# Kernel optimization log

Measured on AMD Instinct MI355X. Metric: run time of the kernel, lower is better.

The kernel has to match this reference:

```python
import jax, jax.numpy as jnp
import numpy as np

B, S, D, H = 2, 2048, 1024, 16
DEPTH = D // H

def setup_inputs() -> dict:
    key = jax.random.key(0)
    ks = jax.random.split(key, 6)
    sc = 0.02
    return {
        "x": jax.random.normal(ks[0], (B, S, D), dtype=jnp.float32),
        "mask": jnp.ones((S, S), dtype=jnp.int32),
        "wq": jax.random.normal(ks[1], (D, D), dtype=jnp.float32) * sc,
        "bq": jnp.zeros((D,), dtype=jnp.float32),
        "wk": jax.random.normal(ks[2], (D, D), dtype=jnp.float32) * sc,
        "bk": jnp.zeros((D,), dtype=jnp.float32),
        "wv": jax.random.normal(ks[3], (D, D), dtype=jnp.float32) * sc,
        "bv": jnp.zeros((D,), dtype=jnp.float32),
        "wo": jax.random.normal(ks[4], (D, D), dtype=jnp.float32) * sc,
        "bo": jnp.zeros((D,), dtype=jnp.float32),
    }

def _split_heads(t):
    # [B,S,D] -> [B,H,S,depth]
    b, s, _ = t.shape
    return t.reshape(b, s, H, DEPTH).transpose(0, 2, 1, 3)

def reference(x, mask, wq, bq, wk, bk, wv, bv, wo, bo):
    q = _split_heads(x @ wq + bq)
    k = _split_heads(x @ wk + bk)
    v = _split_heads(x @ wv + bv)
    scale = 1.0 / jnp.sqrt(jnp.asarray(DEPTH, x.dtype))
    scores = jnp.einsum('bhqd,bhkd->bhqk', q, k) * scale
    # Faithful to original: band_part(ones,-1,0) is the LOWER triangle
    # (incl. diagonal), and it is ADDED times -1e9 -> lower triangle masked.
    s_len = mask.shape[0]
    tri = jnp.tril(jnp.ones((s_len, s_len), dtype=x.dtype))
    scores = scores + tri * (-1e9)
    attn = jax.nn.softmax(scores, axis=-1)  # dropout is identity at inference
    out = jnp.einsum('bhqk,bhkd->bhqd', attn, v)
    out = out.transpose(0, 2, 1, 3).reshape(x.shape[0], -1, D)
    return out @ wo + bo
```

## Files before the change

### kernel.cpp

```cpp
#include <hip/hip_runtime.h>
#include <hip/hip_bf16.h>


using bf16   = __bf16;
using bf16x2 = __attribute__((ext_vector_type(2))) __bf16;
using bf16x4 = __attribute__((ext_vector_type(4))) __bf16;
using bf16x8 = __attribute__((ext_vector_type(8))) __bf16;
using f32x4  = __attribute__((ext_vector_type(4))) float;
using uintx2 = __attribute__((ext_vector_type(2))) unsigned int;
using uintx4 = __attribute__((ext_vector_type(4))) unsigned int;

__device__ __forceinline__ void load_lds16(const void* g, void* l) {
  __builtin_amdgcn_global_load_lds(
      (const __attribute__((address_space(1))) void*)g,
      (__attribute__((address_space(3))) void*)l, 16, 0, 0);
}

__device__ __forceinline__ unsigned int packbf(float a, float b) {
  bf16x2 v;
  v[0] = (bf16)a;
  v[1] = (bf16)b;
  return __builtin_bit_cast(unsigned int, v);
}

__device__ __forceinline__ void xchg_p(unsigned int u, unsigned int v, int hi,
                                       unsigned int& f, unsigned int& s) {
#if __has_builtin(__builtin_amdgcn_permlane32_swap) && \
    __has_builtin(__builtin_amdgcn_permlane16_swap)
  uintx2 ab = __builtin_amdgcn_permlane32_swap(u, v, false, false);
  uintx2 fs = __builtin_amdgcn_permlane16_swap(ab[0], ab[1], false, false);
  f = fs[0];
  s = fs[1];
#else
  unsigned int a = (hi < 2) ? u : (unsigned int)__shfl_xor((int)v, 32);
  unsigned int b = (hi < 2) ? (unsigned int)__shfl_xor((int)u, 32) : v;
  unsigned int a16 = (unsigned int)__shfl_xor((int)a, 16);
  unsigned int b16 = (unsigned int)__shfl_xor((int)b, 16);
  f = (hi & 1) ? b16 : a;
  s = (hi & 1) ? b : a16;
#endif
}

__global__ __launch_bounds__(256) void prep_kernel(
    const float* __restrict__ x, bf16* __restrict__ xb,
    const float* __restrict__ wq, const float* __restrict__ wk,
    const float* __restrict__ wv, const float* __restrict__ wo,
    bf16* __restrict__ wT) {
  const int t = threadIdx.x;
  int bid = blockIdx.x;
  if (bid < 4096) {
    const int i = (bid * 256 + t) * 4;
    const float4 v = *(const float4*)(x + i);
    bf16x4 o;
    o[0] = (bf16)v.x; o[1] = (bf16)v.y; o[2] = (bf16)v.z; o[3] = (bf16)v.w;
    *(bf16x4*)(xb + i) = o;
    return;
  }
  bid -= 4096;
  const int sel = bid >> 8;
  const float* w = (sel == 0) ? wq : (sel == 1) ? wk : (sel == 2) ? wv : wo;
  bf16* out = wT + (size_t)sel * 1048576;
  __shared__ float tile[64][65];
  const int n0 = (bid & 15) * 64;
  const int k0 = ((bid >> 4) & 15) * 64;
#pragma unroll
  for (int p = 0; p < 4; ++p) {
    const int row = p * 16 + (t >> 4);
    const int c4  = (t & 15) * 4;
    const float4 v = *(const float4*)&w[(size_t)(k0 + row) * 1024 + n0 + c4];
    tile[row][c4 + 0] = v.x; tile[row][c4 + 1] = v.y;
    tile[row][c4 + 2] = v.z; tile[row][c4 + 3] = v.w;
  }
  __syncthreads();
#pragma unroll
  for (int p = 0; p < 4; ++p) {
    const int rn = p * 16 + (t >> 4);
    const int c4 = (t & 15) * 4;
    bf16x4 o;
#pragma unroll
    for (int j = 0; j < 4; ++j) o[j] = (bf16)tile[c4 + j][rn];
    *(bf16x4*)&out[(size_t)(n0 + rn) * 1024 + k0 + c4] = o;
  }
}

template <int MODE>
__global__ __launch_bounds__(256, 2) void gemm_bt(
    const bf16* __restrict__ A, const bf16* __restrict__ Bt,
    const float* __restrict__ bias0, const float* __restrict__ bias1,
    const float* __restrict__ bias2, bf16* __restrict__ qf,
    bf16* __restrict__ kf, bf16* __restrict__ vt, float* __restrict__ fout,
    int Nblocks) {
  __shared__ __align__(16) char smem[32768];
  char* sA = smem;
  char* sB = smem + 16384;
  const int tid = threadIdx.x;
  const int lane = tid & 63;
  const int w = tid >> 6;
  const int wm = w >> 1, wn = w & 1;
  const int bid = blockIdx.x;
  const int m0 = (bid / Nblocks) * 128;
  const int n0 = (bid % Nblocks) * 128;

  const char* Ab = (const char*)A;
  const char* Bb = (const char*)Bt;
  size_t srcA[4], srcB[4];
#pragma unroll
  for (int it = 0; it < 4; ++it) {
    const int o = it * 4096 + tid * 16;
    const int r = o >> 7;
    const int cg = ((o >> 4) & 7) ^ (r & 7);
    srcA[it] = (size_t)(m0 + r) * 2048 + cg * 16;
    srcB[it] = (size_t)(n0 + r) * 2048 + cg * 16;
  }

  f32x4 acc[4][4] = {};

  for (int kt = 0; kt < 16; ++kt) {
    const size_t kb = (size_t)kt * 128;
#pragma unroll
    for (int it = 0; it < 4; ++it) {
      load_lds16(Ab + srcA[it] + kb, sA + it * 4096 + w * 1024);
      load_lds16(Bb + srcB[it] + kb, sB + it * 4096 + w * 1024);
    }
    asm volatile("s_waitcnt vmcnt(0)" ::: "memory");
    __syncthreads();
#pragma unroll
    for (int ks = 0; ks < 2; ++ks) {
      bf16x8 aF[4], bF[4];
      const int g = (lane >> 4) + 4 * ks;
#pragma unroll
      for (int i = 0; i < 4; ++i) {
        const int ra = wm * 64 + i * 16 + (lane & 15);
        aF[i] = *(const bf16x8*)(sA + ra * 128 + ((g ^ (ra & 7)) << 4));
        const int rb = wn * 64 + i * 16 + (lane & 15);
        bF[i] = *(const bf16x8*)(sB + rb * 128 + ((g ^ (rb & 7)) << 4));
      }
#pragma unroll
      for (int mi = 0; mi < 4; ++mi)
#pragma unroll
        for (int ni = 0; ni < 4; ++ni)
          acc[mi][ni] = __builtin_amdgcn_mfma_f32_16x16x32_bf16(
              aF[mi], bF[ni], acc[mi][ni], 0, 0, 0);
    }
    __syncthreads();
  }

  const int cn = lane & 15;
  const int gq = lane >> 4;
#pragma unroll
  for (int mi = 0; mi < 4; ++mi) {
#pragma unroll
    for (int ni = 0; ni < 4; ++ni) {
      const int n  = n0 + wn * 64 + ni * 16 + cn;
      const int mb = m0 + wm * 64 + mi * 16 + 4 * gq;
      const f32x4 v = acc[mi][ni];
      if (MODE == 0) {
        const float bias =
            (n < 1024) ? bias0[n] : ((n < 2048) ? bias1[n - 1024] : bias2[n - 2048]);
        if (n < 2048) {
          bf16* dst = (n < 1024) ? qf : kf;
          const int nn = n & 1023;
#pragma unroll
          for (int j = 0; j < 4; ++j)
            dst[(size_t)(mb + j) * 1024 + nn] = (bf16)(v[j] + bias);
        } else {
          const int nn = n - 2048;
          const int hh = nn >> 6, dd = nn & 63;
          const int bb = mb >> 11, ss = mb & 2047;
          bf16x4 pk;
#pragma unroll
          for (int j = 0; j < 4; ++j) pk[j] = (bf16)(v[j] + bias);
          *(bf16x4*)(vt + ((size_t)((bb * 16 + hh) * 64 + dd) * 2048 + ss)) = pk;
        }
      } else {
        const float bias = bias0[n];
#pragma unroll
        for (int j = 0; j < 4; ++j)
          fout[(size_t)(mb + j) * 1024 + n] = v[j] + bias;
      }
    }
  }
}

__global__ __launch_bounds__(256, 2) void attn_kernel(
    const bf16* __restrict__ qf, const bf16* __restrict__ kf,
    const bf16* __restrict__ vt, bf16* __restrict__ ao) {
  __shared__ __align__(16) char smem[32768];

  const int tid  = threadIdx.x;
  const int lane = tid & 63;
  const int hi   = lane >> 4;
  const int qlo  = lane & 15;
  const int w    = tid >> 6;
  const int ti = blockIdx.x >> 5;
  const int jq = (ti < 8) ? ti : 23 - ti;
  const int bh = blockIdx.x & 31;
  const int b = bh >> 4, h = bh & 15;

  const char* kbase = (const char*)kf + ((size_t)b * 2048) * 2048 + h * 128;
  const char* vbase = (const char*)vt + (size_t)bh * 262144;
  const char* qbb   = (const char*)qf + ((size_t)b * 2048) * 2048 + h * 128;

  const int sr  = tid >> 3;
  const int scg = (tid & 7) ^ (sr & 7);

  bf16x8 onesB;
#pragma unroll
  for (int i = 0; i < 8; ++i) onesB[i] = (bf16)1.0f;

  const int q0 = jq * 128;
  const int qb = q0 + w * 32;

  bf16x8 qA[2][2];
#pragma unroll
  for (int nt = 0; nt < 2; ++nt) {
    const char* qrow = qbb + (size_t)(qb + 16 * nt + qlo) * 2048;
#pragma unroll
    for (int ks = 0; ks < 2; ++ks) {
      qA[nt][ks] = *(const bf16x8*)(qrow + ks * 64 + hi * 16);
#pragma unroll
      for (int i = 0; i < 8; ++i)
        qA[nt][ks][i] = (bf16)(0.125f * (float)qA[nt][ks][i]);
    }
  }

  float m[2] = {-1e30f, -1e30f};
  f32x4 lacc[2] = {};
  f32x4 O[2][4] = {};

  const int nt_tiles = (2048 - q0) >> 6;

  {
    char* dK = smem + w * 1024;
    char* dV = smem + 16384 + w * 1024;
#pragma unroll
    for (int p = 0; p < 2; ++p) {
      load_lds16(kbase + (size_t)(q0 + sr + 32 * p) * 2048 + scg * 16,
                 dK + p * 4096);
      load_lds16(vbase + (size_t)(sr + 32 * p) * 4096 + (size_t)q0 * 2 +
                     scg * 16,
                 dV + p * 4096);
    }
  }
  __syncthreads();

  for (int it = 0; it < nt_tiles; ++it) {
    const int cur = it & 1;

    if (it + 1 < nt_tiles) {
      const int kn = q0 + it * 64 + 64;
      char* dK = smem + (cur ^ 1) * 8192 + w * 1024;
      char* dV = smem + 16384 + (cur ^ 1) * 8192 + w * 1024;
#pragma unroll
      for (int p = 0; p < 2; ++p) {
        load_lds16(kbase + (size_t)(kn + sr + 32 * p) * 2048 + scg * 16,
                   dK + p * 4096);
        load_lds16(vbase + (size_t)(sr + 32 * p) * 4096 + (size_t)kn * 2 +
                       scg * 16,
                   dV + p * 4096);
      }
    }
    const char* bK = smem + cur * 8192;
    const char* bV = smem + 16384 + cur * 8192;

    f32x4 sc[2][4] = {};
#pragma unroll
    for (int ks = 0; ks < 2; ++ks) {
      const int g = hi + 4 * ks;
#pragma unroll
      for (int t = 0; t < 4; ++t) {
        const int rk = t * 16 + qlo;
        const bf16x8 kF =
            *(const bf16x8*)(bK + rk * 128 + ((g ^ (rk & 7)) << 4));
        sc[0][t] = __builtin_amdgcn_mfma_f32_16x16x32_bf16(kF, qA[0][ks],
                                                           sc[0][t], 0, 0, 0);
        sc[1][t] = __builtin_amdgcn_mfma_f32_16x16x32_bf16(kF, qA[1][ks],
                                                           sc[1][t], 0, 0, 0);
      }
    }

    if (it < 2) {
      const int k0t = q0 + it * 64;
#pragma unroll
      for (int nt = 0; nt < 2; ++nt)
#pragma unroll
        for (int t = 0; t < 4; ++t)
#pragma unroll
          for (int j = 0; j < 4; ++j) {
            const int kk = k0t + t * 16 + 4 * hi + j;
            const int qq = qb + 16 * nt + qlo;
            if (kk <= qq) sc[nt][t][j] = -1e30f;
          }
    }

    float tm[2];
#pragma unroll
    for (int nt = 0; nt < 2; ++nt) {
      float v = sc[nt][0][0];
#pragma unroll
      for (int t = 0; t < 4; ++t)
#pragma unroll
        for (int j = 0; j < 4; ++j) v = fmaxf(v, sc[nt][t][j]);
      v = fmaxf(v, __shfl_xor(v, 16));
      v = fmaxf(v, __shfl_xor(v, 32));
      tm[nt] = v;
    }

    const bool grew = (tm[0] - m[0] > 8.0f) || (tm[1] - m[1] > 8.0f);
    if (__any(grew)) {
#pragma unroll
      for (int nt = 0; nt < 2; ++nt) {
        const float mn = fmaxf(m[nt], tm[nt]);
        const float al = __expf(m[nt] - mn);
        m[nt] = mn;
#pragma unroll
        for (int j = 0; j < 4; ++j) {
          const float alj = __shfl(al, 4 * hi + j);
          lacc[nt][j] *= alj;
#pragma unroll
          for (int dt = 0; dt < 4; ++dt) O[nt][dt][j] *= alj;
        }
      }
    }

    bf16x8 pA[2][2];
#pragma unroll
    for (int nt = 0; nt < 2; ++nt) {
      unsigned int W[4][2];
#pragma unroll
      for (int t = 0; t < 4; ++t)
#pragma unroll
        for (int p = 0; p < 2; ++p)
          W[t][p] = packbf(__expf(sc[nt][t][2 * p] - m[nt]),
                           __expf(sc[nt][t][2 * p + 1] - m[nt]));
#pragma unroll
      for (int ks = 0; ks < 2; ++ks) {
        uintx4 w4;
#pragma unroll
        for (int p = 0; p < 2; ++p) {
          unsigned int f, s;
          xchg_p(W[2 * ks][p], W[2 * ks + 1][p], hi, f, s);
          w4[p] = f;
          w4[2 + p] = s;
        }
        pA[nt][ks] = __builtin_bit_cast(bf16x8, w4);
        lacc[nt] = __builtin_amdgcn_mfma_f32_16x16x32_bf16(pA[nt][ks], onesB,
                                                           lacc[nt], 0, 0, 0);
      }
    }

#pragma unroll
    for (int ks = 0; ks < 2; ++ks) {
      const int g = hi + 4 * ks;
#pragma unroll
      for (int dt = 0; dt < 4; ++dt) {
        const int rv = dt * 16 + qlo;
        const bf16x8 vF =
            *(const bf16x8*)(bV + rv * 128 + ((g ^ (rv & 7)) << 4));
        O[0][dt] = __builtin_amdgcn_mfma_f32_16x16x32_bf16(pA[0][ks], vF,
                                                           O[0][dt], 0, 0, 0);
        O[1][dt] = __builtin_amdgcn_mfma_f32_16x16x32_bf16(pA[1][ks], vF,
                                                           O[1][dt], 0, 0, 0);
      }
    }
    __syncthreads();
  }

#pragma unroll
  for (int nt = 0; nt < 2; ++nt)
#pragma unroll
    for (int j = 0; j < 4; ++j) {
      const float linv = (lacc[nt][j] > 0.f) ? 1.f / lacc[nt][j] : 0.f;
      const int qg = qb + 16 * nt + 4 * hi + j;
#pragma unroll
      for (int dt = 0; dt < 4; ++dt)
        ao[(size_t)(b * 2048 + qg) * 1024 + h * 64 + dt * 16 + qlo] =
            (bf16)(O[nt][dt][j] * linv);
    }
}

__global__ __launch_bounds__(256) void vmean_kernel(const bf16* __restrict__ vt,
                                                    bf16* __restrict__ ao) {
  const int tid = threadIdx.x;
  const int lane = tid & 63, w = tid >> 6;
  const int gw = blockIdx.x * 4 + w;
  const int bh = gw >> 6, d = gw & 63;
  const int b = bh >> 4, h = bh & 15;
  const bf16x8* p = (const bf16x8*)(vt + (size_t)gw * 2048 + lane * 32);
  float s = 0.f;
#pragma unroll
  for (int i = 0; i < 4; ++i) {
    const bf16x8 v = p[i];
#pragma unroll
    for (int j = 0; j < 8; ++j) s += (float)v[j];
  }
  for (int off = 1; off < 64; off <<= 1) s += __shfl_xor(s, off);
  if (lane == 0)
    ao[(size_t)(b * 2048 + 2047) * 1024 + h * 64 + d] = (bf16)(s * (1.f / 2048.f));
}

extern "C" void kernel_launch(void* const* d_in, const int* in_sizes, int n_in,
                              void* d_out, int out_size, void* d_ws,
                              size_t ws_size, hipStream_t stream) {
  const float* x  = (const float*)d_in[0];
  const float* wq = (const float*)d_in[2];
  const float* bq = (const float*)d_in[3];
  const float* wk = (const float*)d_in[4];
  const float* bk = (const float*)d_in[5];
  const float* wv = (const float*)d_in[6];
  const float* bv = (const float*)d_in[7];
  const float* wo = (const float*)d_in[8];
  const float* bo = (const float*)d_in[9];
  float* out = (float*)d_out;

  if (ws_size < (size_t)25165824 * 2) return;

  bf16* ws    = (bf16*)d_ws;
  bf16* xb    = ws;
  bf16* wqkvT = xb + 4194304;
  bf16* woT   = wqkvT + 3145728;
  bf16* qfp   = woT + 1048576;
  bf16* kfp   = qfp + 4194304;
  bf16* vtp   = kfp + 4194304;
  bf16* aop   = vtp + 4194304;

  prep_kernel<<<5120, 256, 0, stream>>>(x, xb, wq, wk, wv, wo, wqkvT);

  gemm_bt<0><<<32 * 24, 256, 0, stream>>>(xb, wqkvT, bq, bk, bv, qfp, kfp, vtp,
                                          nullptr, 24);
  attn_kernel<<<512, 256, 0, stream>>>(qfp, kfp, vtp, aop);
  vmean_kernel<<<512, 256, 0, stream>>>(vtp, aop);
  gemm_bt<1><<<32 * 8, 256, 0, stream>>>(aop, woT, bo, nullptr, nullptr, nullptr,
                                         nullptr, nullptr, out, 8);
}
```

Before: 110.2 us.

## Triple-buffer K/V tiles in attention with two-ahead prefetch and partial vmcnt waits

Changes the attention kernel's K/V shared-memory staging from double to triple buffering. It prefetches the tile two iterations ahead and uses explicit s_waitcnt vmcnt(4) plus a raw barrier, so only the next tile's loads must land before proceeding. This hides more global-load latency, at the cost of LDS growing from 32KB to 48KB per block. The larger LDS could limit occupancy against the 2-blocks-per-CU launch bound.

```diff
diff --git a/kernel.cpp b/kernel.cpp
--- a/kernel.cpp
+++ b/kernel.cpp
@@ -185,7 +185,7 @@
 __global__ __launch_bounds__(256, 2) void attn_kernel(
     const bf16* __restrict__ qf, const bf16* __restrict__ kf,
     const bf16* __restrict__ vt, bf16* __restrict__ ao) {
-  __shared__ __align__(16) char smem[32768];
+  __shared__ __align__(16) char smem[49152];
 
   const int tid  = threadIdx.x;
   const int lane = tid & 63;
@@ -230,38 +230,38 @@
 
   const int nt_tiles = (2048 - q0) >> 6;
 
-  {
-    char* dK = smem + w * 1024;
-    char* dV = smem + 16384 + w * 1024;
+  auto STAGE = [&](int kt, int bufi) {
+    char* dK = smem + bufi * 16384 + w * 1024;
+    char* dV = smem + bufi * 16384 + 8192 + w * 1024;
+    const int kn = q0 + kt * 64;
 #pragma unroll
     for (int p = 0; p < 2; ++p) {
-      load_lds16(kbase + (size_t)(q0 + sr + 32 * p) * 2048 + scg * 16,
+      load_lds16(kbase + (size_t)(kn + sr + 32 * p) * 2048 + scg * 16,
                  dK + p * 4096);
-      load_lds16(vbase + (size_t)(sr + 32 * p) * 4096 + (size_t)q0 * 2 +
+      load_lds16(vbase + (size_t)(sr + 32 * p) * 4096 + (size_t)kn * 2 +
                      scg * 16,
                  dV + p * 4096);
     }
-  }
-  __syncthreads();
-
+  };
+
+  STAGE(0, 0);
+  if (nt_tiles > 1) {
+    STAGE(1, 1);
+    asm volatile("s_waitcnt vmcnt(4)" ::: "memory");
+  } else {
+    asm volatile("s_waitcnt vmcnt(0)" ::: "memory");
+  }
+  __builtin_amdgcn_s_barrier();
+
+  int cur = 0;
   for (int it = 0; it < nt_tiles; ++it) {
-    const int cur = it & 1;
-
-    if (it + 1 < nt_tiles) {
-      const int kn = q0 + it * 64 + 64;
-      char* dK = smem + (cur ^ 1) * 8192 + w * 1024;
-      char* dV = smem + 16384 + (cur ^ 1) * 8192 + w * 1024;
-#pragma unroll
-      for (int p = 0; p < 2; ++p) {
-        load_lds16(kbase + (size_t)(kn + sr + 32 * p) * 2048 + scg * 16,
-                   dK + p * 4096);
-        load_lds16(vbase + (size_t)(sr + 32 * p) * 4096 + (size_t)kn * 2 +
-                       scg * 16,
-                   dV + p * 4096);
-      }
-    }
-    const char* bK = smem + cur * 8192;
-    const char* bV = smem + 16384 + cur * 8192;
+    if (it + 2 < nt_tiles) {
+      int bufi = cur + 2;
+      if (bufi >= 3) bufi -= 3;
+      STAGE(it + 2, bufi);
+    }
+    const char* bK = smem + cur * 16384;
+    const char* bV = smem + cur * 16384 + 8192;
 
     f32x4 sc[2][4] = {};
 #pragma unroll
@@ -363,7 +363,16 @@
                                                            O[1][dt], 0, 0, 0);
       }
     }
-    __syncthreads();
+
+    if (it + 1 < nt_tiles) {
+      if (it + 2 < nt_tiles)
+        asm volatile("s_waitcnt vmcnt(4)" ::: "memory");
+      else
+        asm volatile("s_waitcnt vmcnt(0)" ::: "memory");
+      __builtin_amdgcn_s_barrier();
+    }
+    ++cur;
+    if (cur >= 3) cur = 0;
   }
 
 #pragma unroll
```

New measurement: 112.0 us. No clear change (+1.6%).

## Split long causal attention tiles into two KV halves with a combine pass

Applied to the files above, without the earlier changes.

Replaces the one-block-per-query-tile attention grid with a table-driven schedule of 768 blocks. The longest query tiles have their KV range split across two blocks, which write unnormalised partial outputs plus per-row max and sum. A new combine kernel merges the two halves. Occupancy is also raised to 3 blocks per CU. The goal is to balance work across CUs and cut tail latency, at the cost of an extra kernel launch, partial-result traffic, and reusing the xb workspace as scratch.

```diff
diff --git a/kernel.cpp b/kernel.cpp
--- a/kernel.cpp
+++ b/kernel.cpp
@@ -182,20 +182,49 @@
   }
 }
 
-__global__ __launch_bounds__(256, 2) void attn_kernel(
+__global__ __launch_bounds__(256, 3) void attn_kernel(
     const bf16* __restrict__ qf, const bf16* __restrict__ kf,
-    const bf16* __restrict__ vt, bf16* __restrict__ ao) {
+    const bf16* __restrict__ vt, bf16* __restrict__ ao,
+    bf16* __restrict__ o2buf, float* __restrict__ mlbuf) {
   __shared__ __align__(16) char smem[32768];
+
+  const unsigned int TAB[24] = {
+      0u | (0u << 8)  | (16u << 16) | (1u << 24),
+      0u | (16u << 8) | (32u << 16) | (2u << 24),
+      1u | (2u << 8)  | (17u << 16) | (1u << 24),
+      1u | (17u << 8) | (32u << 16) | (2u << 24),
+      2u | (4u << 8)  | (18u << 16) | (1u << 24),
+      2u | (18u << 8) | (32u << 16) | (2u << 24),
+      3u | (6u << 8)  | (19u << 16) | (1u << 24),
+      4u | (8u << 8)  | (20u << 16) | (1u << 24),
+      8u | (16u << 8) | (32u << 16) | (0u << 24),
+      9u | (18u << 8) | (32u << 16) | (0u << 24),
+      3u | (19u << 8) | (32u << 16) | (2u << 24),
+      5u | (10u << 8) | (21u << 16) | (1u << 24),
+      5u | (21u << 8) | (32u << 16) | (2u << 24),
+      6u | (12u << 8) | (22u << 16) | (1u << 24),
+      4u | (20u << 8) | (32u << 16) | (2u << 24),
+      10u | (20u << 8) | (32u << 16) | (0u << 24),
+      15u | (30u << 8) | (32u << 16) | (0u << 24),
+      14u | (28u << 8) | (32u << 16) | (0u << 24),
+      13u | (26u << 8) | (32u << 16) | (0u << 24),
+      12u | (24u << 8) | (32u << 16) | (0u << 24),
+      7u | (14u << 8) | (23u << 16) | (1u << 24),
+      6u | (22u << 8) | (32u << 16) | (2u << 24),
+      7u | (23u << 8) | (32u << 16) | (2u << 24),
+      11u | (22u << 8) | (32u << 16) | (0u << 24)};
 
   const int tid  = threadIdx.x;
   const int lane = tid & 63;
   const int hi   = lane >> 4;
   const int qlo  = lane & 15;
   const int w    = tid >> 6;
-  const int ti = blockIdx.x >> 5;
-  const int jq = (ti < 8) ? ti : 23 - ti;
+  const int u  = blockIdx.x >> 5;
   const int bh = blockIdx.x & 31;
   const int b = bh >> 4, h = bh & 15;
+  const unsigned int ent = TAB[u];
+  const int jq = ent & 255, kbeg = (ent >> 8) & 255, kend = (ent >> 16) & 255;
+  const int mode = ent >> 24;
 
   const char* kbase = (const char*)kf + ((size_t)b * 2048) * 2048 + h * 128;
   const char* vbase = (const char*)vt + (size_t)bh * 262144;
@@ -228,38 +257,28 @@
   f32x4 lacc[2] = {};
   f32x4 O[2][4] = {};
 
-  const int nt_tiles = (2048 - q0) >> 6;
-
-  {
-    char* dK = smem + w * 1024;
-    char* dV = smem + 16384 + w * 1024;
+  auto STAGE = [&](int kt, int bufi) {
+    char* dK = smem + bufi * 8192 + w * 1024;
+    char* dV = smem + 16384 + bufi * 8192 + w * 1024;
+    const int kn = kt * 64;
 #pragma unroll
     for (int p = 0; p < 2; ++p) {
-      load_lds16(kbase + (size_t)(q0 + sr + 32 * p) * 2048 + scg * 16,
+      load_lds16(kbase + (size_t)(kn + sr + 32 * p) * 2048 + scg * 16,
                  dK + p * 4096);
-      load_lds16(vbase + (size_t)(sr + 32 * p) * 4096 + (size_t)q0 * 2 +
+      load_lds16(vbase + (size_t)(sr + 32 * p) * 4096 + (size_t)kn * 2 +
                      scg * 16,
                  dV + p * 4096);
     }
-  }
+  };
+
+  STAGE(kbeg, 0);
   __syncthreads();
 
-  for (int it = 0; it < nt_tiles; ++it) {
-    const int cur = it & 1;
-
-    if (it + 1 < nt_tiles) {
-      const int kn = q0 + it * 64 + 64;
-      char* dK = smem + (cur ^ 1) * 8192 + w * 1024;
-      char* dV = smem + 16384 + (cur ^ 1) * 8192 + w * 1024;
-#pragma unroll
-      for (int p = 0; p < 2; ++p) {
-        load_lds16(kbase + (size_t)(kn + sr + 32 * p) * 2048 + scg * 16,
-                   dK + p * 4096);
-        load_lds16(vbase + (size_t)(sr + 32 * p) * 4096 + (size_t)kn * 2 +
-                       scg * 16,
-                   dV + p * 4096);
-      }
-    }
+  for (int kt = kbeg; kt < kend; ++kt) {
+    const int cur = (kt - kbeg) & 1;
+
+    if (kt + 1 < kend) STAGE(kt + 1, cur ^ 1);
+
     const char* bK = smem + cur * 8192;
     const char* bV = smem + 16384 + cur * 8192;
 
@@ -279,8 +298,8 @@
       }
     }
 
-    if (it < 2) {
-      const int k0t = q0 + it * 64;
+    if (kt * 64 < q0 + 128) {
+      const int k0t = kt * 64;
 #pragma unroll
       for (int nt = 0; nt < 2; ++nt)
 #pragma unroll
@@ -366,17 +385,83 @@
     __syncthreads();
   }
 
-#pragma unroll
-  for (int nt = 0; nt < 2; ++nt)
-#pragma unroll
-    for (int j = 0; j < 4; ++j) {
-      const float linv = (lacc[nt][j] > 0.f) ? 1.f / lacc[nt][j] : 0.f;
-      const int qg = qb + 16 * nt + 4 * hi + j;
-#pragma unroll
-      for (int dt = 0; dt < 4; ++dt)
-        ao[(size_t)(b * 2048 + qg) * 1024 + h * 64 + dt * 16 + qlo] =
-            (bf16)(O[nt][dt][j] * linv);
-    }
+  if (mode == 0) {
+#pragma unroll
+    for (int nt = 0; nt < 2; ++nt)
+#pragma unroll
+      for (int j = 0; j < 4; ++j) {
+        const float linv = (lacc[nt][j] > 0.f) ? 1.f / lacc[nt][j] : 0.f;
+        const int qg = qb + 16 * nt + 4 * hi + j;
+#pragma unroll
+        for (int dt = 0; dt < 4; ++dt)
+          ao[(size_t)(b * 2048 + qg) * 1024 + h * 64 + dt * 16 + qlo] =
+              (bf16)(O[nt][dt][j] * linv);
+      }
+  } else {
+    const int qtbh = jq * 32 + bh;
+    const int slot = mode - 1;
+#pragma unroll
+    for (int nt = 0; nt < 2; ++nt)
+#pragma unroll
+      for (int j = 0; j < 4; ++j) {
+        const int r = w * 32 + 16 * nt + 4 * hi + j;
+#pragma unroll
+        for (int dt = 0; dt < 4; ++dt) {
+          const bf16 vv = (bf16)O[nt][dt][j];
+          if (mode == 1)
+            ao[(size_t)(b * 2048 + q0 + r) * 1024 + h * 64 + dt * 16 + qlo] = vv;
+          else
+            o2buf[(size_t)(qtbh * 128 + r) * 64 + dt * 16 + qlo] = vv;
+        }
+      }
+    if (qlo == 0) {
+#pragma unroll
+      for (int nt = 0; nt < 2; ++nt)
+#pragma unroll
+        for (int j = 0; j < 4; ++j)
+          mlbuf[((qtbh * 2 + slot) * 2 + 1) * 128 + (w * 32 + 16 * nt + 4 * hi + j)] =
+              lacc[nt][j];
+    }
+    if (hi == 0) {
+#pragma unroll
+      for (int nt = 0; nt < 2; ++nt)
+        mlbuf[((qtbh * 2 + slot) * 2 + 0) * 128 + (w * 32 + 16 * nt + qlo)] =
+            m[nt];
+    }
+  }
+}
+
+__global__ __launch_bounds__(256) void combine_kernel(
+    const bf16* __restrict__ o2buf, const float* __restrict__ mlbuf,
+    bf16* __restrict__ ao) {
+  const int qtbh = blockIdx.x;
+  const int jq = qtbh >> 5, bh = qtbh & 31;
+  const int b = bh >> 4, h = bh & 15;
+  const int t = threadIdx.x;
+  const int r = t >> 1;
+  const int c0 = (t & 1) * 32;
+
+  const float m1 = mlbuf[((qtbh * 2 + 0) * 2 + 0) * 128 + r];
+  const float l1 = mlbuf[((qtbh * 2 + 0) * 2 + 1) * 128 + r];
+  const float m2 = mlbuf[((qtbh * 2 + 1) * 2 + 0) * 128 + r];
+  const float l2 = mlbuf[((qtbh * 2 + 1) * 2 + 1) * 128 + r];
+  const float M  = fmaxf(m1, m2);
+  const float w1 = __expf(m1 - M), w2 = __expf(m2 - M);
+  const float denom = w1 * l1 + w2 * l2;
+  const float linv = (denom > 0.f) ? 1.f / denom : 0.f;
+
+  bf16* arow = ao + ((size_t)(b * 2048 + jq * 128 + r) * 1024 + h * 64 + c0);
+  const bf16* o2row = o2buf + ((size_t)(qtbh * 128 + r) * 64 + c0);
+#pragma unroll
+  for (int i = 0; i < 4; ++i) {
+    const bf16x8 o1 = *(const bf16x8*)(arow + i * 8);
+    const bf16x8 o2 = *(const bf16x8*)(o2row + i * 8);
+    bf16x8 o;
+#pragma unroll
+    for (int j = 0; j < 8; ++j)
+      o[j] = (bf16)((w1 * (float)o1[j] + w2 * (float)o2[j]) * linv);
+    *(bf16x8*)(arow + i * 8) = o;
+  }
 }
 
 __global__ __launch_bounds__(256) void vmean_kernel(const bf16* __restrict__ vt,
@@ -424,12 +509,16 @@
   bf16* vtp   = kfp + 4194304;
   bf16* aop   = vtp + 4194304;
 
+  bf16*  o2buf = xb;
+  float* mlbuf = (float*)(xb + 2097152);
+
   prep_kernel<<<5120, 256, 0, stream>>>(x, xb, wq, wk, wv, wo, wqkvT);
 
   gemm_bt<0><<<32 * 24, 256, 0, stream>>>(xb, wqkvT, bq, bk, bv, qfp, kfp, vtp,
                                           nullptr, 24);
-  attn_kernel<<<512, 256, 0, stream>>>(qfp, kfp, vtp, aop);
+  attn_kernel<<<768, 256, 0, stream>>>(qfp, kfp, vtp, aop, o2buf, mlbuf);
   vmean_kernel<<<512, 256, 0, stream>>>(vtp, aop);
+  combine_kernel<<<256, 256, 0, stream>>>(o2buf, mlbuf, aop);
   gemm_bt<1><<<32 * 8, 256, 0, stream>>>(aop, woT, bo, nullptr, nullptr, nullptr,
                                          nullptr, nullptr, out, 8);
 }
```

Measured after the change: 106.9 us. -3.0%, faster.
